# Kernel optimization log

Measured on AMD Instinct MI355X. Metric: run time of the kernel, lower is better.

## Reference

```python
import jax, jax.numpy as jnp
import numpy as np

N = 524288
D_IN = 14
HID = 128
LAT = 5
VOCAB = 256
BETA = 0.25


def setup_inputs() -> dict:
    key = jax.random.key(0)
    ks = jax.random.split(key, 12)
    s = lambda fi: 1.0 / np.sqrt(fi)
    inp = {
        "x": jax.random.normal(ks[0], (N, D_IN), jnp.float32),
        "enc_w1": jax.random.uniform(ks[1], (D_IN, HID), jnp.float32, -s(D_IN), s(D_IN)),
        "enc_b1": jnp.zeros((HID,), jnp.float32),
        "enc_w2": jax.random.uniform(ks[2], (HID, HID), jnp.float32, -s(HID), s(HID)),
        "enc_b2": jnp.zeros((HID,), jnp.float32),
        "enc_w3": jax.random.uniform(ks[3], (HID, LAT), jnp.float32, -s(HID), s(HID)),
        "enc_b3": jnp.zeros((LAT,), jnp.float32),
        "emb": jax.random.uniform(ks[4], (VOCAB, LAT), jnp.float32, -1.0 / VOCAB, 1.0 / VOCAB),
        "dec_w1": jax.random.uniform(ks[5], (LAT, HID), jnp.float32, -s(LAT), s(LAT)),
        "dec_b1": jnp.zeros((HID,), jnp.float32),
        "dec_w2": jax.random.uniform(ks[6], (HID, D_IN), jnp.float32, -s(HID), s(HID)),
        "dec_b2": jnp.zeros((D_IN,), jnp.float32),
    }
    return inp


def reference(x, enc_w1, enc_b1, enc_w2, enc_b2, enc_w3, enc_b3, emb,
              dec_w1, dec_b1, dec_w2, dec_b2):
    # encoder MLP: [N,14] -> [N,5]
    h = jax.nn.relu(x @ enc_w1 + enc_b1)
    h = jax.nn.relu(h @ enc_w2 + enc_b2)
    quant_input = h @ enc_w3 + enc_b3  # [N, LAT]

    # squared distances to codebook (argmin identical to cdist argmin)
    d2 = (jnp.sum(quant_input * quant_input, axis=1, keepdims=True)
          - 2.0 * quant_input @ emb.T
          + jnp.sum(emb * emb, axis=1)[None, :])  # [N, VOCAB]
    min_idx = jnp.argmin(d2, axis=1)                       # [N]
    min_encoding_indices = min_idx[:, None]                # [N, 1]
    min_encodings = jax.nn.one_hot(min_idx, VOCAB, dtype=quant_input.dtype)  # [N, VOCAB]

    # gather via one-hot matmul, as in the original
    quant_out = min_encodings @ emb                        # [N, LAT]

    e_mean = jnp.mean(min_encodings, axis=0)
    perplexity = jnp.exp(-jnp.sum(e_mean * jnp.log(e_mean + 1e-10)))

    sg = jax.lax.stop_gradient
    code_book_loss = jnp.mean((sg(quant_input) - quant_out) ** 2)
    commitment_loss = jnp.mean((quant_input - sg(quant_out)) ** 2)
    quant_loss = code_book_loss + BETA * commitment_loss

    # straight-through estimator
    quant_out = quant_input + sg(quant_out - quant_input)

    # decoder MLP: [N,5] -> [N,14]
    h = jax.nn.relu(quant_out @ dec_w1 + dec_b1)
    output = h @ dec_w2 + dec_b2
    return output, quant_loss, perplexity, min_encodings, min_encoding_indices
```

## Files before the change

### kernel.cpp

```cpp
#include <hip/hip_runtime.h>
#include <cstdint>
#include <cstddef>

#define NROWS 524288
#define DIN 14
#define HID 128
#define LAT 5
#define VOCAB 256
#define BR 128
#define NT 512
#define HS 132

#define FENCE(v) asm volatile("" : "+v"(v))

static constexpr size_t LOSS_OFF = 7340032;
static constexpr size_t PERP_OFF = 7340033;
static constexpr size_t OH_OFF   = 7340034;
static constexpr size_t IDX_OFF  = 141557762;

static constexpr int OFF_W2   = 0;
static constexpr int OFF_H    = 16384;
static constexpr int OFF_W1T  = 33280;
static constexpr int OFF_IDX  = 33280;
static constexpr int OFF_HIST = 33408;
static constexpr int OFF_RED  = 33664;
static constexpr int OFF_Q    = 33680;
static constexpr int OFF_QE4  = 34320;
static constexpr int OFF_QE1  = 34832;
static constexpr int OFF_B1   = 35328;
static constexpr int OFF_B2   = 35456;
static constexpr int OFF_W3T  = 35584;
static constexpr int OFF_B3   = 36244;
static constexpr int OFF_EMB8 = 36252;
static constexpr int OFF_DW1  = 38300;
static constexpr int OFF_DB1  = 38940;
static constexpr int OFF_DW2T = 39068;
static constexpr int OFF_DB2  = 40916;
static constexpr int SMEM_FLOATS = 40932;
static constexpr int SMEM_BYTES  = SMEM_FLOATS * 4;
static_assert(SMEM_BYTES <= 160*1024, "LDS over budget");
static_assert(OFF_QE4 + 512 <= OFF_QE1 && OFF_QE1 + 128 <= 35328, "union overflow");
static_assert((OFF_H % 4) == 0 && (OFF_W1T % 4) == 0 && (OFF_W3T % 4) == 0 &&
              (OFF_EMB8 % 4) == 0 && (OFF_DW2T % 4) == 0 && (OFF_QE4 % 4) == 0, "align");

__global__ __launch_bounds__(NT, 1)
void vqvae_main(const float* __restrict__ x,
                const float* __restrict__ ew1, const float* __restrict__ eb1,
                const float* __restrict__ ew2, const float* __restrict__ eb2,
                const float* __restrict__ ew3, const float* __restrict__ eb3,
                const float* __restrict__ emb,
                const float* __restrict__ dw1, const float* __restrict__ db1,
                const float* __restrict__ dw2, const float* __restrict__ db2,
                float* __restrict__ out,
                double* __restrict__ loss_sum,
                unsigned int* __restrict__ hist_g)
{
    #pragma clang fp contract(off)

    extern __shared__ float smem[];
    float* s_w2   = smem + OFF_W2;
    float* s_h    = smem + OFF_H;
    float* s_w1t  = smem + OFF_W1T;
    float* s_b1   = smem + OFF_B1;
    float* s_b2   = smem + OFF_B2;
    float* s_w3t  = smem + OFF_W3T;
    float* s_b3   = smem + OFF_B3;
    float* s_emb8 = smem + OFF_EMB8;
    float* s_dw1  = smem + OFF_DW1;
    float* s_db1  = smem + OFF_DB1;
    float* s_dw2t = smem + OFF_DW2T;
    float* s_db2  = smem + OFF_DB2;
    float* s_q    = smem + OFF_Q;
    float* s_qe4  = smem + OFF_QE4;
    float* s_qe1  = smem + OFF_QE1;
    int*   s_idx  = reinterpret_cast<int*>(smem + OFF_IDX);
    unsigned int* s_hist = reinterpret_cast<unsigned int*>(smem + OFF_HIST);
    float* s_red  = smem + OFF_RED;

    const int tid = threadIdx.x;
    const int r_base = blockIdx.x * BR;

    for (int i = tid; i < HID*HID/4; i += NT)
        reinterpret_cast<float4*>(s_w2)[i] = reinterpret_cast<const float4*>(ew2)[i];
    for (int i = tid; i < DIN*HID; i += NT) {
        const int k = i >> 7, c = i & 127;
        s_w1t[c*16 + k] = ew1[i];
    }
    for (int i = tid; i < VOCAB*LAT; i += NT) {
        const int v = i / 5, k = i - 5*v;
        s_emb8[v*8 + k] = emb[i];
    }
    for (int i = tid; i < HID*LAT; i += NT) {
        const int k = i / 5, c = i - 5*k;
        s_w3t[c*132 + k] = ew3[i];
    }
    for (int i = tid; i < LAT*HID; i += NT) s_dw1[i] = dw1[i];
    for (int i = tid; i < HID*DIN; i += NT) {
        const int k = i / 14, c = i - 14*k;
        s_dw2t[c*132 + k] = dw2[i];
    }
    if (tid < HID) { s_b1[tid] = eb1[tid]; s_b2[tid] = eb2[tid]; s_db1[tid] = db1[tid]; }
    if (tid < LAT) s_b3[tid] = eb3[tid];
    if (tid < DIN) s_db2[tid] = db2[tid];
    __syncthreads();

    if (tid < VOCAB) {
        const float* e8 = &s_emb8[tid*8];
        float p0 = e8[0]*e8[0];
        float p1 = e8[1]*e8[1];
        float p2 = e8[2]*e8[2];
        float p3 = e8[3]*e8[3];
        float p4 = e8[4]*e8[4];
        float e = p0 + p1; FENCE(e);
        e = e + p2; FENCE(e);
        e = e + p3; FENCE(e);
        e = e + p4; FENCE(e);
        s_emb8[tid*8 + 5] = e;
    }

    {
        const int r  = tid >> 2;
        const int q4 = tid & 3;
        const float* xrow = x + (size_t)(r_base + r) * DIN;
        float xr[DIN];
        #pragma unroll
        for (int k = 0; k < DIN; k += 2) {
            float2 v = *reinterpret_cast<const float2*>(xrow + k);
            xr[k] = v.x; xr[k+1] = v.y;
        }
        for (int cc = 0; cc < HID/4; ++cc) {
            const int c = q4 + 4*cc;
            const float4 wq0 = *reinterpret_cast<const float4*>(&s_w1t[c*16 + 0]);
            const float4 wq1 = *reinterpret_cast<const float4*>(&s_w1t[c*16 + 4]);
            const float4 wq2 = *reinterpret_cast<const float4*>(&s_w1t[c*16 + 8]);
            const float4 wq3 = *reinterpret_cast<const float4*>(&s_w1t[c*16 + 12]);
            const float w[14] = {wq0.x,wq0.y,wq0.z,wq0.w, wq1.x,wq1.y,wq1.z,wq1.w,
                                 wq2.x,wq2.y,wq2.z,wq2.w, wq3.x,wq3.y};
            float s = 0.f;
            #pragma unroll
            for (int k = 0; k < DIN; ++k) { s = fmaf(xr[k], w[k], s); FENCE(s); }
            s = s + s_b1[c]; FENCE(s);
            s_h[r*HS + c] = fmaxf(s, 0.f);
        }
    }
    __syncthreads();

    {
        const int trow = tid >> 4;
        const int tcol = tid & 15;
        const int r0 = trow * 4, c0 = tcol * 8;
        float accE[4][8], accO[4][8];
        #pragma unroll
        for (int i = 0; i < 4; ++i)
            #pragma unroll
            for (int j = 0; j < 8; ++j) { accE[i][j] = 0.f; accO[i][j] = 0.f; }

        for (int k = 0; k < HID; k += 2) {
            float hvE[4], hvO[4];
            #pragma unroll
            for (int i = 0; i < 4; ++i) {
                const float2 hp = *reinterpret_cast<const float2*>(&s_h[(r0+i)*HS + k]);
                hvE[i] = hp.x; hvO[i] = hp.y;
            }
            float4 waE = *reinterpret_cast<const float4*>(&s_w2[k*HID + c0]);
            float4 wbE = *reinterpret_cast<const float4*>(&s_w2[k*HID + c0 + 4]);
            float4 waO = *reinterpret_cast<const float4*>(&s_w2[(k+1)*HID + c0]);
            float4 wbO = *reinterpret_cast<const float4*>(&s_w2[(k+1)*HID + c0 + 4]);
            float wE[8] = {waE.x, waE.y, waE.z, waE.w, wbE.x, wbE.y, wbE.z, wbE.w};
            float wO[8] = {waO.x, waO.y, waO.z, waO.w, wbO.x, wbO.y, wbO.z, wbO.w};
            #pragma unroll
            for (int i = 0; i < 4; ++i)
                #pragma unroll
                for (int j = 0; j < 8; ++j) {
                    accE[i][j] = fmaf(hvE[i], wE[j], accE[i][j]); FENCE(accE[i][j]);
                    accO[i][j] = fmaf(hvO[i], wO[j], accO[i][j]); FENCE(accO[i][j]);
                }
        }
        __syncthreads();
        #pragma unroll
        for (int i = 0; i < 4; ++i)
            #pragma unroll
            for (int j = 0; j < 8; ++j) {
                const int c = c0 + j;
                float s = accE[i][j] + accO[i][j]; FENCE(s);
                s = s + s_b2[c]; FENCE(s);
                s_h[(r0+i)*HS + c] = fmaxf(s, 0.f);
            }
    }
    __syncthreads();

    for (int oi = tid; oi < BR*LAT; oi += NT) {
        const int r = oi / LAT;
        const int c = oi - r*LAT;
        float s = 0.f;
        for (int kq = 0; kq < HID; kq += 4) {
            const float4 hq = *reinterpret_cast<const float4*>(&s_h[r*HS + kq]);
            const float4 wq = *reinterpret_cast<const float4*>(&s_w3t[c*132 + kq]);
            s = fmaf(hq.x, wq.x, s); FENCE(s);
            s = fmaf(hq.y, wq.y, s); FENCE(s);
            s = fmaf(hq.z, wq.z, s); FENCE(s);
            s = fmaf(hq.w, wq.w, s); FENCE(s);
        }
        s = s + s_b3[c]; FENCE(s);
        s_q[r*LAT + c] = s;
    }
    if (tid < VOCAB) s_hist[tid] = 0u;
    __syncthreads();

    float loss_local = 0.f;
    {
        const int r  = tid >> 2;
        const int q4 = tid & 3;
        float qv[LAT];
        #pragma unroll
        for (int k = 0; k < LAT; ++k) qv[k] = s_q[r*LAT + k];

        float qp0 = qv[0]*qv[0];
        float qp1 = qv[1]*qv[1];
        float qp2 = qv[2]*qv[2];
        float qp3 = qv[3]*qv[3];
        float qp4 = qv[4]*qv[4];
        float qq = qp0 + qp1; FENCE(qq);
        qq = qq + qp2; FENCE(qq);
        qq = qq + qp3; FENCE(qq);
        qq = qq + qp4; FENCE(qq);

        float bd = 3.4e38f; int bv = VOCAB;
        for (int ii = 0; ii < VOCAB/4; ++ii) {
            const int v = q4 + 4*ii;
            const float4 elo = *reinterpret_cast<const float4*>(&s_emb8[v*8]);
            const float4 ehi = *reinterpret_cast<const float4*>(&s_emb8[v*8 + 4]);
            float dot = 0.f;
            dot = fmaf(qv[4], ehi.x, dot); FENCE(dot);
            dot = fmaf(qv[3], elo.w, dot); FENCE(dot);
            dot = fmaf(qv[2], elo.z, dot); FENCE(dot);
            dot = fmaf(qv[1], elo.y, dot); FENCE(dot);
            dot = fmaf(qv[0], elo.x, dot); FENCE(dot);
            float twodot = 2.0f * dot; FENCE(twodot);
            float t1 = qq - twodot; FENCE(t1);
            float sc = t1 + ehi.y; FENCE(sc);
            const bool better = (sc < bd) || (sc == bd && v < bv);
            bd = better ? sc : bd;
            bv = better ? v  : bv;
        }
        #pragma unroll
        for (int m = 1; m <= 2; m <<= 1) {
            const float od = __shfl_xor(bd, m);
            const int   ov = __shfl_xor(bv, m);
            const bool better = (od < bd) || (od == bd && ov < bv);
            bd = better ? od : bd;
            bv = better ? ov : bv;
        }
        if (q4 == 0) {
            s_idx[r] = bv;
            atomicAdd(&s_hist[bv], 1u);
            float ls = 0.f;
            #pragma unroll
            for (int k = 0; k < LAT; ++k) {
                const float d = qv[k] - s_emb8[bv*8 + k];
                ls = fmaf(d, d, ls);
            }
            loss_local = ls;
            #pragma unroll
            for (int k = 0; k < 4; ++k) {
                const float ev = s_emb8[bv*8 + k];
                s_qe4[r*4 + k] = qv[k] + (ev - qv[k]);
            }
            {
                const float ev = s_emb8[bv*8 + 4];
                s_qe1[r] = qv[4] + (ev - qv[4]);
            }
        }
    }

    {
        float s = loss_local;
        #pragma unroll
        for (int off = 32; off > 0; off >>= 1) s += __shfl_down(s, off);
        if ((tid & 63) == 0) s_red[tid >> 6] = s;
    }
    __syncthreads();
    if (tid == 0) {
        float s = 0.f;
        #pragma unroll
        for (int w = 0; w < NT/64; ++w) s += s_red[w];
        atomicAdd(loss_sum, (double)s);
    }
    if (tid < VOCAB) {
        const unsigned c = s_hist[tid];
        if (c) atomicAdd(&hist_g[tid], c);
    }

    {
        float* oh = out + OH_OFF;
        const int rr0 = tid >> 7;
        const int c0  = (tid & 127) * 2;
        for (int it = 0; it < BR/4; ++it) {
            const int r = it*4 + rr0;
            const int best = s_idx[r];
            float2 v;
            v.x = (c0     == best) ? 1.f : 0.f;
            v.y = (c0 + 1 == best) ? 1.f : 0.f;
            *reinterpret_cast<float2*>(oh + (size_t)(r_base + r)*VOCAB + c0) = v;
        }
        if (tid < BR) out[IDX_OFF + r_base + tid] = (float)s_idx[tid];
    }

    {
        const int r  = tid >> 2;
        const int q4 = tid & 3;
        const float4 qlo = *reinterpret_cast<const float4*>(&s_qe4[r*4]);
        const float qe4v = s_qe1[r];
        for (int cc = 0; cc < HID/4; ++cc) {
            const int c = q4 + 4*cc;
            float s = 0.f;
            s = fmaf(qlo.x, s_dw1[0*HID + c], s);
            s = fmaf(qlo.y, s_dw1[1*HID + c], s);
            s = fmaf(qlo.z, s_dw1[2*HID + c], s);
            s = fmaf(qlo.w, s_dw1[3*HID + c], s);
            s = fmaf(qe4v,  s_dw1[4*HID + c], s);
            s_h[r*HS + c] = fmaxf(s + s_db1[c], 0.f);
        }
    }
    __syncthreads();

    for (int oi = tid; oi < BR*DIN; oi += NT) {
        const int r = oi / DIN;
        const int c = oi - r*DIN;
        float s = 0.f;
        for (int kq = 0; kq < HID; kq += 4) {
            const float4 hq = *reinterpret_cast<const float4*>(&s_h[r*HS + kq]);
            const float4 wq = *reinterpret_cast<const float4*>(&s_dw2t[c*132 + kq]);
            s = fmaf(hq.x, wq.x, s);
            s = fmaf(hq.y, wq.y, s);
            s = fmaf(hq.z, wq.z, s);
            s = fmaf(hq.w, wq.w, s);
        }
        out[(size_t)r_base*DIN + oi] = s + s_db2[c];
    }
}

__global__ void vq_init(double* loss, unsigned int* hist)
{
    if (threadIdx.x == 0) *loss = 0.0;
    if (threadIdx.x < VOCAB) hist[threadIdx.x] = 0u;
}

__global__ void vq_final(const double* __restrict__ loss,
                         const unsigned int* __restrict__ hist,
                         float* __restrict__ out)
{
    #pragma clang fp contract(off)
    __shared__ float red[4];
    const int t = threadIdx.x;
    const float em = (float)hist[t] / (float)NROWS;
    float s = em * logf(em + 1e-10f);
    #pragma unroll
    for (int off = 32; off > 0; off >>= 1) s += __shfl_down(s, off);
    if ((t & 63) == 0) red[t >> 6] = s;
    __syncthreads();
    if (t == 0) {
        const float tot = red[0] + red[1] + red[2] + red[3];
        out[PERP_OFF] = expf(-tot);
        out[LOSS_OFF] = 1.25f * (float)(*loss / (double)((size_t)NROWS * LAT));
    }
}

extern "C" void kernel_launch(void* const* d_in, const int* in_sizes, int n_in,
                              void* d_out, int out_size, void* d_ws, size_t ws_size,
                              hipStream_t stream)
{
    const float* x   = (const float*)d_in[0];
    const float* ew1 = (const float*)d_in[1];
    const float* eb1 = (const float*)d_in[2];
    const float* ew2 = (const float*)d_in[3];
    const float* eb2 = (const float*)d_in[4];
    const float* ew3 = (const float*)d_in[5];
    const float* eb3 = (const float*)d_in[6];
    const float* emb = (const float*)d_in[7];
    const float* dw1 = (const float*)d_in[8];
    const float* db1 = (const float*)d_in[9];
    const float* dw2 = (const float*)d_in[10];
    const float* db2 = (const float*)d_in[11];
    float* out = (float*)d_out;

    double* loss = (double*)d_ws;
    unsigned int* hist = (unsigned int*)((char*)d_ws + 8);

    hipFuncSetAttribute(reinterpret_cast<const void*>(vqvae_main),
                        hipFuncAttributeMaxDynamicSharedMemorySize, SMEM_BYTES);

    vq_init<<<1, 256, 0, stream>>>(loss, hist);
    vqvae_main<<<NROWS / BR, NT, SMEM_BYTES, stream>>>(
        x, ew1, eb1, ew2, eb2, ew3, eb3, emb, dw1, db1, dw2, db2,
        out, loss, hist);
    vq_final<<<1, 256, 0, stream>>>(loss, hist, out);
}
```

Measured before the change: 1.200 ms.

## Halve row tile and split W2 staging to fit two blocks per CU

Reduces rows per block from 128 to 64 and reorganizes LDS so that encoder W2 is staged in two 64-row halves through a shared buffer aliased with the later codebook/decoder weights, cutting LDS to under 80KB. Launch bounds are raised so more blocks can be resident per CU, aiming to hide global-memory latency of the large one-hot writes. It adds extra barriers and doubles total weight reloads from global/L2 across twice as many blocks, and re-maps thread-to-row partitions (8 threads per row).

```diff
diff --git a/kernel.cpp b/kernel.cpp
--- a/kernel.cpp
+++ b/kernel.cpp
@@ -7,7 +7,7 @@
 #define HID 128
 #define LAT 5
 #define VOCAB 256
-#define BR 128
+#define BR 64
 #define NT 512
 #define HS 132
 
@@ -18,32 +18,31 @@
 static constexpr size_t OH_OFF   = 7340034;
 static constexpr size_t IDX_OFF  = 141557762;
 
-static constexpr int OFF_W2   = 0;
-static constexpr int OFF_H    = 16384;
-static constexpr int OFF_W1T  = 33280;
-static constexpr int OFF_IDX  = 33280;
-static constexpr int OFF_HIST = 33408;
-static constexpr int OFF_RED  = 33664;
-static constexpr int OFF_Q    = 33680;
-static constexpr int OFF_QE4  = 34320;
-static constexpr int OFF_QE1  = 34832;
-static constexpr int OFF_B1   = 35328;
-static constexpr int OFF_B2   = 35456;
-static constexpr int OFF_W3T  = 35584;
-static constexpr int OFF_B3   = 36244;
-static constexpr int OFF_EMB8 = 36252;
-static constexpr int OFF_DW1  = 38300;
-static constexpr int OFF_DB1  = 38940;
-static constexpr int OFF_DW2T = 39068;
-static constexpr int OFF_DB2  = 40916;
-static constexpr int SMEM_FLOATS = 40932;
+static constexpr int OFF_WBUF = 0;
+static constexpr int OFF_EMB8 = 0;
+static constexpr int OFF_W3T  = 2048;
+static constexpr int OFF_DW1T = 2712;
+static constexpr int OFF_DW2T = 3736;
+static constexpr int OFF_B3   = 5584;
+static constexpr int OFF_DB1  = 5592;
+static constexpr int OFF_DB2  = 5720;
+static constexpr int OFF_Q    = 5736;
+static constexpr int OFF_QE4  = 6056;
+static constexpr int OFF_QE1  = 6312;
+static constexpr int OFF_IDX  = 6376;
+static constexpr int OFF_HIST = 6440;
+static constexpr int OFF_RED  = 6696;
+static constexpr int OFF_H    = 8192;
+static constexpr int OFF_W1T  = 16640;
+static constexpr int OFF_B1   = 19200;
+static constexpr int OFF_B2   = 19328;
+static constexpr int SMEM_FLOATS = 19456;
 static constexpr int SMEM_BYTES  = SMEM_FLOATS * 4;
-static_assert(SMEM_BYTES <= 160*1024, "LDS over budget");
-static_assert(OFF_QE4 + 512 <= OFF_QE1 && OFF_QE1 + 128 <= 35328, "union overflow");
-static_assert((OFF_H % 4) == 0 && (OFF_W1T % 4) == 0 && (OFF_W3T % 4) == 0 &&
-              (OFF_EMB8 % 4) == 0 && (OFF_DW2T % 4) == 0 && (OFF_QE4 % 4) == 0, "align");
-
-__global__ __launch_bounds__(NT, 1)
+static_assert(SMEM_BYTES <= 80*1024, "need <=80KB for 2 blocks/CU");
+static_assert((OFF_W3T%4)==0 && (OFF_DW1T%4)==0 && (OFF_DW2T%4)==0 &&
+              (OFF_QE4%4)==0 && (OFF_H%4)==0 && (OFF_W1T%4)==0, "align");
+
+__global__ __launch_bounds__(NT, 4)
 void vqvae_main(const float* __restrict__ x,
                 const float* __restrict__ ew1, const float* __restrict__ eb1,
                 const float* __restrict__ ew2, const float* __restrict__ eb2,
@@ -58,17 +57,17 @@
     #pragma clang fp contract(off)
 
     extern __shared__ float smem[];
-    float* s_w2   = smem + OFF_W2;
+    float* s_wbuf = smem + OFF_WBUF;
     float* s_h    = smem + OFF_H;
     float* s_w1t  = smem + OFF_W1T;
     float* s_b1   = smem + OFF_B1;
     float* s_b2   = smem + OFF_B2;
+    float* s_emb8 = smem + OFF_EMB8;
     float* s_w3t  = smem + OFF_W3T;
+    float* s_dw1t = smem + OFF_DW1T;
+    float* s_dw2t = smem + OFF_DW2T;
     float* s_b3   = smem + OFF_B3;
-    float* s_emb8 = smem + OFF_EMB8;
-    float* s_dw1  = smem + OFF_DW1;
     float* s_db1  = smem + OFF_DB1;
-    float* s_dw2t = smem + OFF_DW2T;
     float* s_db2  = smem + OFF_DB2;
     float* s_q    = smem + OFF_Q;
     float* s_qe4  = smem + OFF_QE4;
@@ -80,28 +79,121 @@
     const int tid = threadIdx.x;
     const int r_base = blockIdx.x * BR;
 
-    for (int i = tid; i < HID*HID/4; i += NT)
-        reinterpret_cast<float4*>(s_w2)[i] = reinterpret_cast<const float4*>(ew2)[i];
-    for (int i = tid; i < DIN*HID; i += NT) {
-        const int k = i >> 7, c = i & 127;
-        s_w1t[c*16 + k] = ew1[i];
-    }
-    for (int i = tid; i < VOCAB*LAT; i += NT) {
-        const int v = i / 5, k = i - 5*v;
-        s_emb8[v*8 + k] = emb[i];
-    }
-    for (int i = tid; i < HID*LAT; i += NT) {
-        const int k = i / 5, c = i - 5*k;
-        s_w3t[c*132 + k] = ew3[i];
-    }
-    for (int i = tid; i < LAT*HID; i += NT) s_dw1[i] = dw1[i];
-    for (int i = tid; i < HID*DIN; i += NT) {
-        const int k = i / 14, c = i - 14*k;
-        s_dw2t[c*132 + k] = dw2[i];
-    }
-    if (tid < HID) { s_b1[tid] = eb1[tid]; s_b2[tid] = eb2[tid]; s_db1[tid] = db1[tid]; }
-    if (tid < LAT) s_b3[tid] = eb3[tid];
-    if (tid < DIN) s_db2[tid] = db2[tid];
+    {
+        float4* wb4 = reinterpret_cast<float4*>(s_wbuf);
+        const float4* w2g = reinterpret_cast<const float4*>(ew2);
+        for (int i = tid; i < 2048; i += NT) wb4[i] = w2g[i];
+        for (int i = tid; i < DIN*HID; i += NT) {
+            const int k = i >> 7, c = i & 127;
+            s_w1t[c*20 + k] = ew1[i];
+        }
+        if (tid < HID) { s_b1[tid] = eb1[tid]; s_b2[tid] = eb2[tid]; }
+    }
+    __syncthreads();
+
+    {
+        const int r  = tid >> 3;
+        const int q8 = tid & 7;
+        const float* xrow = x + (size_t)(r_base + r) * DIN;
+        float xr[DIN];
+        #pragma unroll
+        for (int k = 0; k < DIN; k += 2) {
+            float2 v = *reinterpret_cast<const float2*>(xrow + k);
+            xr[k] = v.x; xr[k+1] = v.y;
+        }
+        for (int cc = 0; cc < HID/8; ++cc) {
+            const int c = q8 + 8*cc;
+            const float4 wq0 = *reinterpret_cast<const float4*>(&s_w1t[c*20 + 0]);
+            const float4 wq1 = *reinterpret_cast<const float4*>(&s_w1t[c*20 + 4]);
+            const float4 wq2 = *reinterpret_cast<const float4*>(&s_w1t[c*20 + 8]);
+            const float4 wq3 = *reinterpret_cast<const float4*>(&s_w1t[c*20 + 12]);
+            const float w[14] = {wq0.x,wq0.y,wq0.z,wq0.w, wq1.x,wq1.y,wq1.z,wq1.w,
+                                 wq2.x,wq2.y,wq2.z,wq2.w, wq3.x,wq3.y};
+            float s = 0.f;
+            #pragma unroll
+            for (int k = 0; k < DIN; ++k) { s = fmaf(xr[k], w[k], s); FENCE(s); }
+            s = s + s_b1[c]; FENCE(s);
+            s_h[r*HS + c] = fmaxf(s, 0.f);
+        }
+    }
+    __syncthreads();
+
+    {
+        const int trow = tid >> 4;
+        const int tcol = tid & 15;
+        const int r0 = trow * 2, c0 = tcol * 8;
+        float accE[2][8], accO[2][8];
+        #pragma unroll
+        for (int i = 0; i < 2; ++i)
+            #pragma unroll
+            for (int j = 0; j < 8; ++j) { accE[i][j] = 0.f; accO[i][j] = 0.f; }
+
+        #pragma unroll 1
+        for (int pass = 0; pass < 2; ++pass) {
+            const int kbase = pass * 64;
+            for (int kk = 0; kk < 64; kk += 2) {
+                float hvE[2], hvO[2];
+                #pragma unroll
+                for (int i = 0; i < 2; ++i) {
+                    const float2 hp = *reinterpret_cast<const float2*>(&s_h[(r0+i)*HS + kbase + kk]);
+                    hvE[i] = hp.x; hvO[i] = hp.y;
+                }
+                float4 waE = *reinterpret_cast<const float4*>(&s_wbuf[kk*HID + c0]);
+                float4 wbE = *reinterpret_cast<const float4*>(&s_wbuf[kk*HID + c0 + 4]);
+                float4 waO = *reinterpret_cast<const float4*>(&s_wbuf[(kk+1)*HID + c0]);
+                float4 wbO = *reinterpret_cast<const float4*>(&s_wbuf[(kk+1)*HID + c0 + 4]);
+                float wE[8] = {waE.x, waE.y, waE.z, waE.w, wbE.x, wbE.y, wbE.z, wbE.w};
+                float wO[8] = {waO.x, waO.y, waO.z, waO.w, wbO.x, wbO.y, wbO.z, wbO.w};
+                #pragma unroll
+                for (int i = 0; i < 2; ++i)
+                    #pragma unroll
+                    for (int j = 0; j < 8; ++j) {
+                        accE[i][j] = fmaf(hvE[i], wE[j], accE[i][j]); FENCE(accE[i][j]);
+                        accO[i][j] = fmaf(hvO[i], wO[j], accO[i][j]); FENCE(accO[i][j]);
+                    }
+            }
+            __syncthreads();
+            if (pass == 0) {
+                float4* wb4 = reinterpret_cast<float4*>(s_wbuf);
+                const float4* w2g = reinterpret_cast<const float4*>(ew2);
+                for (int i = tid; i < 2048; i += NT) wb4[i] = w2g[i + 2048];
+                __syncthreads();
+            }
+        }
+        #pragma unroll
+        for (int i = 0; i < 2; ++i)
+            #pragma unroll
+            for (int j = 0; j < 8; ++j) {
+                const int c = c0 + j;
+                float s = accE[i][j] + accO[i][j]; FENCE(s);
+                s = s + s_b2[c]; FENCE(s);
+                s_h[(r0+i)*HS + c] = fmaxf(s, 0.f);
+            }
+    }
+    __syncthreads();
+
+    {
+        for (int i = tid; i < VOCAB*LAT; i += NT) {
+            const int v = i / 5, k = i - 5*v;
+            s_emb8[v*8 + k] = emb[i];
+        }
+        for (int i = tid; i < HID*LAT; i += NT) {
+            const int k = i / 5, c = i - 5*k;
+            s_w3t[c*132 + k] = ew3[i];
+        }
+        for (int i = tid; i < LAT*HID; i += NT) {
+            const int k = i >> 7, c = i & 127;
+            s_dw1t[c*8 + k] = dw1[i];
+        }
+        for (int i = tid; i < HID*DIN; i += NT) {
+            const int k = i / 14, c = i - 14*k;
+            s_dw2t[c*132 + k] = dw2[i];
+        }
+        if (tid < LAT) s_b3[tid] = eb3[tid];
+        if (tid < HID) s_db1[tid] = db1[tid];
+        if (tid < DIN) s_db2[tid] = db2[tid];
+        if (tid < VOCAB) s_hist[tid] = 0u;
+    }
     __syncthreads();
 
     if (tid < VOCAB) {
@@ -117,81 +209,9 @@
         e = e + p4; FENCE(e);
         s_emb8[tid*8 + 5] = e;
     }
-
-    {
-        const int r  = tid >> 2;
-        const int q4 = tid & 3;
-        const float* xrow = x + (size_t)(r_base + r) * DIN;
-        float xr[DIN];
-        #pragma unroll
-        for (int k = 0; k < DIN; k += 2) {
-            float2 v = *reinterpret_cast<const float2*>(xrow + k);
-            xr[k] = v.x; xr[k+1] = v.y;
-        }
-        for (int cc = 0; cc < HID/4; ++cc) {
-            const int c = q4 + 4*cc;
-            const float4 wq0 = *reinterpret_cast<const float4*>(&s_w1t[c*16 + 0]);
-            const float4 wq1 = *reinterpret_cast<const float4*>(&s_w1t[c*16 + 4]);
-            const float4 wq2 = *reinterpret_cast<const float4*>(&s_w1t[c*16 + 8]);
-            const float4 wq3 = *reinterpret_cast<const float4*>(&s_w1t[c*16 + 12]);
-            const float w[14] = {wq0.x,wq0.y,wq0.z,wq0.w, wq1.x,wq1.y,wq1.z,wq1.w,
-                                 wq2.x,wq2.y,wq2.z,wq2.w, wq3.x,wq3.y};
-            float s = 0.f;
-            #pragma unroll
-            for (int k = 0; k < DIN; ++k) { s = fmaf(xr[k], w[k], s); FENCE(s); }
-            s = s + s_b1[c]; FENCE(s);
-            s_h[r*HS + c] = fmaxf(s, 0.f);
-        }
-    }
-    __syncthreads();
-
-    {
-        const int trow = tid >> 4;
-        const int tcol = tid & 15;
-        const int r0 = trow * 4, c0 = tcol * 8;
-        float accE[4][8], accO[4][8];
-        #pragma unroll
-        for (int i = 0; i < 4; ++i)
-            #pragma unroll
-            for (int j = 0; j < 8; ++j) { accE[i][j] = 0.f; accO[i][j] = 0.f; }
-
-        for (int k = 0; k < HID; k += 2) {
-            float hvE[4], hvO[4];
-            #pragma unroll
-            for (int i = 0; i < 4; ++i) {
-                const float2 hp = *reinterpret_cast<const float2*>(&s_h[(r0+i)*HS + k]);
-                hvE[i] = hp.x; hvO[i] = hp.y;
-            }
-            float4 waE = *reinterpret_cast<const float4*>(&s_w2[k*HID + c0]);
-            float4 wbE = *reinterpret_cast<const float4*>(&s_w2[k*HID + c0 + 4]);
-            float4 waO = *reinterpret_cast<const float4*>(&s_w2[(k+1)*HID + c0]);
-            float4 wbO = *reinterpret_cast<const float4*>(&s_w2[(k+1)*HID + c0 + 4]);
-            float wE[8] = {waE.x, waE.y, waE.z, waE.w, wbE.x, wbE.y, wbE.z, wbE.w};
-            float wO[8] = {waO.x, waO.y, waO.z, waO.w, wbO.x, wbO.y, wbO.z, wbO.w};
-            #pragma unroll
-            for (int i = 0; i < 4; ++i)
-                #pragma unroll
-                for (int j = 0; j < 8; ++j) {
-                    accE[i][j] = fmaf(hvE[i], wE[j], accE[i][j]); FENCE(accE[i][j]);
-                    accO[i][j] = fmaf(hvO[i], wO[j], accO[i][j]); FENCE(accO[i][j]);
-                }
-        }
-        __syncthreads();
-        #pragma unroll
-        for (int i = 0; i < 4; ++i)
-            #pragma unroll
-            for (int j = 0; j < 8; ++j) {
-                const int c = c0 + j;
-                float s = accE[i][j] + accO[i][j]; FENCE(s);
-                s = s + s_b2[c]; FENCE(s);
-                s_h[(r0+i)*HS + c] = fmaxf(s, 0.f);
-            }
-    }
-    __syncthreads();
-
-    for (int oi = tid; oi < BR*LAT; oi += NT) {
-        const int r = oi / LAT;
-        const int c = oi - r*LAT;
+    if (tid < BR*LAT) {
+        const int r = tid / LAT;
+        const int c = tid - r*LAT;
         float s = 0.f;
         for (int kq = 0; kq < HID; kq += 4) {
             const float4 hq = *reinterpret_cast<const float4*>(&s_h[r*HS + kq]);
@@ -204,13 +224,12 @@
         s = s + s_b3[c]; FENCE(s);
         s_q[r*LAT + c] = s;
     }
-    if (tid < VOCAB) s_hist[tid] = 0u;
     __syncthreads();
 
     float loss_local = 0.f;
     {
-        const int r  = tid >> 2;
-        const int q4 = tid & 3;
+        const int r  = tid >> 3;
+        const int q8 = tid & 7;
         float qv[LAT];
         #pragma unroll
         for (int k = 0; k < LAT; ++k) qv[k] = s_q[r*LAT + k];
@@ -226,8 +245,8 @@
         qq = qq + qp4; FENCE(qq);
 
         float bd = 3.4e38f; int bv = VOCAB;
-        for (int ii = 0; ii < VOCAB/4; ++ii) {
-            const int v = q4 + 4*ii;
+        for (int ii = 0; ii < VOCAB/8; ++ii) {
+            const int v = q8 + 8*ii;
             const float4 elo = *reinterpret_cast<const float4*>(&s_emb8[v*8]);
             const float4 ehi = *reinterpret_cast<const float4*>(&s_emb8[v*8 + 4]);
             float dot = 0.f;
@@ -244,14 +263,14 @@
             bv = better ? v  : bv;
         }
         #pragma unroll
-        for (int m = 1; m <= 2; m <<= 1) {
+        for (int m = 1; m <= 4; m <<= 1) {
             const float od = __shfl_xor(bd, m);
             const int   ov = __shfl_xor(bv, m);
             const bool better = (od < bd) || (od == bd && ov < bv);
             bd = better ? od : bd;
             bv = better ? ov : bv;
         }
-        if (q4 == 0) {
+        if (q8 == 0) {
             s_idx[r] = bv;
             atomicAdd(&s_hist[bv], 1u);
             float ls = 0.f;
@@ -307,18 +326,20 @@
     }
 
     {
-        const int r  = tid >> 2;
-        const int q4 = tid & 3;
+        const int r  = tid >> 3;
+        const int q8 = tid & 7;
         const float4 qlo = *reinterpret_cast<const float4*>(&s_qe4[r*4]);
         const float qe4v = s_qe1[r];
-        for (int cc = 0; cc < HID/4; ++cc) {
-            const int c = q4 + 4*cc;
+        for (int cc = 0; cc < HID/8; ++cc) {
+            const int c = q8 + 8*cc;
+            const float4 wq = *reinterpret_cast<const float4*>(&s_dw1t[c*8]);
+            const float w4 = s_dw1t[c*8 + 4];
             float s = 0.f;
-            s = fmaf(qlo.x, s_dw1[0*HID + c], s);
-            s = fmaf(qlo.y, s_dw1[1*HID + c], s);
-            s = fmaf(qlo.z, s_dw1[2*HID + c], s);
-            s = fmaf(qlo.w, s_dw1[3*HID + c], s);
-            s = fmaf(qe4v,  s_dw1[4*HID + c], s);
+            s = fmaf(qlo.x, wq.x, s);
+            s = fmaf(qlo.y, wq.y, s);
+            s = fmaf(qlo.z, wq.z, s);
+            s = fmaf(qlo.w, wq.w, s);
+            s = fmaf(qe4v,  w4,   s);
             s_h[r*HS + c] = fmaxf(s + s_db1[c], 0.f);
         }
     }
```

Measured after the change: 1.072 ms. 10.6% less time.
